# Performance work log

Hardware: AMD Instinct MI355X
Metric: run time of the kernel (lower is better)

Reference implementation:

```python
import jax, jax.numpy as jnp
import numpy as np

V = 100277      # VOCAB_SIZE
SCR = 64        # SCRATCH_SLOTS
STEPS = 8       # MAX_STEPS_LIMIT
H = 8           # num_heads (hard-coded in UniversalReasoner)
NEG = -1e9


def _layernorm(x, s, b, eps=1e-6):
    mu = x.mean(-1, keepdims=True)
    var = ((x - mu) ** 2).mean(-1, keepdims=True)
    return (x - mu) * jax.lax.rsqrt(var + eps) * s + b


def setup_inputs() -> dict:
    key = jax.random.key(0)
    ks = jax.random.split(key, 16)
    D = 1024
    n = lambda k, shape, sc=0.02: jax.random.normal(k, shape, dtype=jnp.float32) * sc
    return {
        "tokens": jax.random.randint(ks[0], (16, 128), 0, V),
        "embed": n(ks[1], (V, D)),
        "time_embed": n(ks[2], (STEPS + 1, D)),
        "scratch": n(ks[3], (1, SCR, D)),
        "wq": n(ks[4], (D, D)), "bq": jnp.zeros((D,), jnp.float32),
        "wk": n(ks[5], (D, D)), "bk": jnp.zeros((D,), jnp.float32),
        "wv": n(ks[6], (D, D)), "bv": jnp.zeros((D,), jnp.float32),
        "wo": n(ks[7], (D, D)), "bo": jnp.zeros((D,), jnp.float32),
        "ln1_s": jnp.ones((D,), jnp.float32), "ln1_b": jnp.zeros((D,), jnp.float32),
        "ln2_s": jnp.ones((D,), jnp.float32), "ln2_b": jnp.zeros((D,), jnp.float32),
        "w1": n(ks[8], (D, 4 * D)), "b1": jnp.zeros((4 * D,), jnp.float32),
        "w2": n(ks[9], (4 * D, D)), "b2": jnp.zeros((D,), jnp.float32),
        "halt_w": n(ks[10], (D, 1)), "halt_b": jnp.zeros((1,), jnp.float32),
        "dec_w": n(ks[11], (D, V)), "dec_b": jnp.zeros((V,), jnp.float32),
    }


def reference(tokens, embed, time_embed, scratch, wq, bq, wk, bk, wv, bv, wo, bo,
              ln1_s, ln1_b, ln2_s, ln2_b, w1, b1, w2, b2, halt_w, halt_b, dec_w, dec_b):
    B, S = tokens.shape
    D = embed.shape[1]
    hd = D // H
    T = S + SCR                     # seq + scratch slots
    scale = hd ** -0.5

    # RoPE caches (matches 10000**(arange(0,hd,2)/hd) in the module)
    inv_freq = 1.0 / 10000.0 ** (jnp.arange(0, hd, 2, dtype=jnp.float32) / hd)
    t = jnp.arange(T, dtype=jnp.float32)
    freqs = jnp.outer(t, inv_freq)              # [T, hd/2]
    sin = jnp.sin(freqs); cos = jnp.cos(freqs)
    sin_ext = jnp.stack([sin, sin], -1).reshape(T, hd)[None, :, None, :]
    cos_ext = jnp.stack([cos, cos], -1).reshape(T, hd)[None, :, None, :]

    # hybrid mask: causal for the seq part, fully-visible rows for scratch tokens
    causal = jnp.tril(jnp.ones((T, T), dtype=bool))
    mask = causal.at[S:, :].set(True)[None, None, :, :]   # [1,1,T,T]

    def rotate(x):  # x: [B,T,H,hd]
        xe, xo = x[..., 0::2], x[..., 1::2]
        xr = jnp.stack([-xo, xe], -1).reshape(x.shape)
        return x * cos_ext + xr * sin_ext

    def block(x):   # one StandardReasoningBlock on [B,T,D]
        h = _layernorm(x, ln1_s, ln1_b)
        q = (h @ wq + bq).reshape(B, T, H, hd)
        k = (h @ wk + bk).reshape(B, T, H, hd)
        v = (h @ wv + bv).reshape(B, T, H, hd)
        q, k = rotate(q), rotate(k)
        logits = jnp.einsum('bshd,bthd->bhst', q, k) * scale
        logits = jnp.where(mask, logits, NEG)
        w = jax.nn.softmax(logits, axis=-1)
        o = jnp.einsum('bhst,bthd->bshd', w, v).reshape(B, T, D)
        x = x + (o @ wo + bo)
        h2 = _layernorm(x, ln2_s, ln2_b)
        x = x + jax.nn.gelu(h2 @ w1 + b1, approximate=True) @ w2 + b2
        return x

    z0 = jnp.concatenate([embed[tokens], jnp.tile(scratch, (B, 1, 1))], axis=1)  # [B,T,D]

    def step(z, i):
        zt = z + time_embed[i][None, None, :]
        nz = block(zt)
        halt = jax.nn.sigmoid((nz[:, S:, :] @ halt_w + halt_b).mean(axis=(1, 2)))  # [B]
        return nz, halt

    final_z, halts = jax.lax.scan(step, z0, jnp.arange(STEPS))   # halts: [STEPS, B]
    logits_out = final_z[:, :S, :] @ dec_w + dec_b               # [B,S,V]
    return logits_out, halts
```

## Files before the change

kernel.cpp:

```cpp
#include <hip/hip_runtime.h>
#include <hip/hip_bf16.h>
#include <math.h>


typedef float  f32x4  __attribute__((ext_vector_type(4)));
typedef __bf16 bf16x8 __attribute__((ext_vector_type(8)));
typedef __bf16 bf16x4 __attribute__((ext_vector_type(4)));

static constexpr int BB   = 16;
static constexpr int S    = 128;
static constexpr int SCR  = 64;
static constexpr int T    = 192;
static constexpr int D    = 1024;
static constexpr int H    = 8;
static constexpr int HD   = 128;
static constexpr int DFF  = 4096;
static constexpr int NSTEP= 8;
static constexpr int V    = 100277;
static constexpr int ROWS = BB * T;
static constexpr int MD   = BB * S;
static constexpr long long LOGITS = (long long)BB * S * V;
static constexpr size_t QSZ = (size_t)BB * H * T * HD;

#define DEV __device__ __forceinline__

DEV void gload16(const __bf16* g, __bf16* l) {
  __builtin_amdgcn_global_load_lds(
      (__attribute__((address_space(1))) void*)(g),
      (__attribute__((address_space(3))) void*)(l), 16, 0, 0);
}

template <int EPI>
__global__ __launch_bounds__(256) void k_gemm(
    const __bf16* __restrict__ A, long long sA, int ldA, int M,
    const __bf16* __restrict__ Bt, long long sB, int ldB, int N, int K,
    const float* __restrict__ bias, void* __restrict__ C, long long sC,
    int ldC, const float* __restrict__ rct, const float* __restrict__ rst) {
  const int bz = blockIdx.z;
  const __bf16* Ab;
  const __bf16* Bb;
  if constexpr (EPI == 4) {
    Ab = A + (size_t)bz * K;
    Bb = Bt + (size_t)bz * K;
  } else {
    Ab = A + (size_t)bz * sA;
    Bb = Bt + (size_t)bz * sB;
  }
  const int tm = blockIdx.y * 128, tn = blockIdx.x * 128;
  const int tid = threadIdx.x;
  const int lane = tid & 63, wv = tid >> 6;
  const int wr = wv >> 1, wc = wv & 1;

  __shared__ __bf16 As[2][128 * 32];
  __shared__ __bf16 Bs[2][128 * 32];

  f32x4 acc[4][4];
#pragma unroll
  for (int m = 0; m < 4; m++)
#pragma unroll
    for (int n = 0; n < 4; n++) acc[m][n] = (f32x4)(0.f);

  const int lrow = lane >> 2;
  const int lcol = (((lane & 3) ^ ((lrow >> 1) & 3)) * 8);
  int arow[2], brow[2];
#pragma unroll
  for (int c2 = 0; c2 < 2; c2++) {
    const int ch = wv * 2 + c2;
    int ar = tm + ch * 16 + lrow; if (ar > M - 1) ar = M - 1;
    int br = tn + ch * 16 + lrow; if (br > N - 1) br = N - 1;
    arow[c2] = ar; brow[c2] = br;
  }

  auto stage = [&](int buf, int kk) {
#pragma unroll
    for (int c2 = 0; c2 < 2; c2++) {
      const int ch = wv * 2 + c2;
      gload16(Ab + (size_t)arow[c2] * ldA + kk + lcol, &As[buf][ch * 512]);
      gload16(Bb + (size_t)brow[c2] * ldB + kk + lcol, &Bs[buf][ch * 512]);
    }
  };

  const int rsl = (((lane >> 4) ^ (((lane & 15) >> 1) & 3)) * 8);
  auto compute = [&](int cur) {
    bf16x8 af[4], bfv[4];
#pragma unroll
    for (int m = 0; m < 4; m++)
      af[m] = *(const bf16x8*)&As[cur][(wr * 64 + m * 16 + (lane & 15)) * 32 + rsl];
#pragma unroll
    for (int n = 0; n < 4; n++)
      bfv[n] = *(const bf16x8*)&Bs[cur][(wc * 64 + n * 16 + (lane & 15)) * 32 + rsl];
    asm volatile("s_waitcnt lgkmcnt(0)" ::: "memory");
    __builtin_amdgcn_sched_barrier(0);
    __builtin_amdgcn_s_barrier();
#pragma unroll
    for (int m = 0; m < 4; m++)
#pragma unroll
      for (int n = 0; n < 4; n++)
        acc[m][n] = __builtin_amdgcn_mfma_f32_16x16x32_bf16(af[m], bfv[n],
                                                            acc[m][n], 0, 0, 0);
  };

  const int niter = K >> 5;
  stage(0, 0);
  for (int it = 0; it < niter - 1; ++it) {
    const int cur = it & 1;
    stage(cur ^ 1, (it + 1) << 5);
    asm volatile("s_waitcnt vmcnt(4)" ::: "memory");
    __builtin_amdgcn_s_barrier();
    compute(cur);
  }
  asm volatile("s_waitcnt vmcnt(0)" ::: "memory");
  __builtin_amdgcn_s_barrier();
  compute((niter - 1) & 1);

  const int r0 = tm + wr * 64, c0 = tn + wc * 64;
  if constexpr (EPI == 5) {
    const int kind = tn >> 10;
#pragma unroll
    for (int n = 0; n < 4; n++) {
      const int c = c0 + n * 16 + (lane & 15);
      const int hh = (c & 1023) >> 7, d = c & 127, jp = d >> 1;
      const float bsv = bias[c];
#pragma unroll
      for (int m = 0; m < 4; m++) {
        const int rb = r0 + m * 16 + ((lane >> 4) << 2);
#pragma unroll
        for (int j = 0; j < 4; j++) {
          const int r = rb + j;
          const float x = acc[m][n][j] + bsv;
          const float xo = __shfl_xor(x, 1);
          const int b = r / T, t = r % T;
          if (kind == 2) {
            ((__bf16*)C)[2 * QSZ + ((size_t)((b * H + hh) * HD + d)) * T + t] =
                (__bf16)x;
          } else {
            const float cs = rct[t * 64 + jp], sn = rst[t * 64 + jp];
            const float o = (c & 1) ? (x * cs + xo * sn) : (x * cs - xo * sn);
            ((__bf16*)C)[(size_t)kind * QSZ +
                         ((size_t)((b * H + hh) * T + t)) * HD + d] = (__bf16)o;
          }
        }
      }
    }
    return;
  }
#pragma unroll
  for (int n = 0; n < 4; n++) {
    const int c = c0 + n * 16 + (lane & 15);
    if (c >= N) continue;
    const float bsv = (bias && (EPI != 4 || bz == 0)) ? bias[c] : 0.f;
#pragma unroll
    for (int m = 0; m < 4; m++) {
      const int rb = r0 + m * 16 + ((lane >> 4) << 2);
#pragma unroll
      for (int j = 0; j < 4; j++) {
        const int r = rb + j;
        if (r >= M) continue;
        float x = acc[m][n][j] + bsv;
        if constexpr (EPI == 3) {
          const int b = bz >> 3, hh = bz & 7;
          ((__bf16*)C)[((size_t)(b * T + r)) * D + hh * HD + c] = (__bf16)x;
        } else if constexpr (EPI == 4) {
          atomicAdd((float*)C + (size_t)r * ldC + c, x);
        } else {
          const size_t idx = (size_t)bz * sC + (size_t)r * ldC + c;
          if constexpr (EPI == 2) {
            const float u = x;
            const float gl =
                0.5f * u * (1.f + tanhf(0.7978845608f * (u + 0.044715f * u * u * u)));
            ((__bf16*)C)[idx] = (__bf16)gl;
          } else if constexpr (EPI == 1) {
            ((float*)C)[idx] += x;
          } else {
            ((float*)C)[idx] = x;
          }
        }
      }
    }
  }
}

static constexpr int DEC_NT = (V + 127) / 128;
static constexpr int DEC_NWG = 16 * DEC_NT;

__global__ __launch_bounds__(256) void k_dec(const __bf16* __restrict__ A,
                                             const __bf16* __restrict__ Bt,
                                             const float* __restrict__ bias,
                                             float* __restrict__ C) {
  const int bid = blockIdx.x;
  const int swz = (bid & 7) * (DEC_NWG / 8) + (bid >> 3);
  const int tm = (swz & 15) * 128, tn = (swz >> 4) * 128;
  const int tid = threadIdx.x;
  const int lane = tid & 63, wv = tid >> 6;
  const int wr = wv >> 1, wc = wv & 1;

  __shared__ __bf16 sAB[2][2][4096];
  float* cbuf = (float*)sAB;

  f32x4 acc[4][4];
#pragma unroll
  for (int m = 0; m < 4; m++)
#pragma unroll
    for (int n = 0; n < 4; n++) acc[m][n] = (f32x4)(0.f);

  const int lrow = lane >> 2;
  const int lcol = (((lane & 3) ^ ((lrow >> 1) & 3)) * 8);
  int arow[2], brow[2];
#pragma unroll
  for (int c2 = 0; c2 < 2; c2++) {
    const int ch = wv * 2 + c2;
    arow[c2] = tm + ch * 16 + lrow;
    int br = tn + ch * 16 + lrow; if (br > V - 1) br = V - 1;
    brow[c2] = br;
  }

  auto stage = [&](int buf, int kk) {
#pragma unroll
    for (int c2 = 0; c2 < 2; c2++) {
      const int ch = wv * 2 + c2;
      gload16(A + (size_t)arow[c2] * D + kk + lcol, &sAB[buf][0][ch * 512]);
      gload16(Bt + (size_t)brow[c2] * D + kk + lcol, &sAB[buf][1][ch * 512]);
    }
  };

  const int rsl = (((lane >> 4) ^ (((lane & 15) >> 1) & 3)) * 8);
  auto compute = [&](int cur) {
    bf16x8 af[4], bfv[4];
#pragma unroll
    for (int m = 0; m < 4; m++)
      af[m] = *(const bf16x8*)&sAB[cur][0][(wr * 64 + m * 16 + (lane & 15)) * 32 + rsl];
#pragma unroll
    for (int n = 0; n < 4; n++)
      bfv[n] = *(const bf16x8*)&sAB[cur][1][(wc * 64 + n * 16 + (lane & 15)) * 32 + rsl];
    asm volatile("s_waitcnt lgkmcnt(0)" ::: "memory");
    __builtin_amdgcn_sched_barrier(0);
    __builtin_amdgcn_s_barrier();
#pragma unroll
    for (int m = 0; m < 4; m++)
#pragma unroll
      for (int n = 0; n < 4; n++)
        acc[m][n] = __builtin_amdgcn_mfma_f32_16x16x32_bf16(af[m], bfv[n],
                                                            acc[m][n], 0, 0, 0);
  };

  stage(0, 0);
  for (int it = 0; it < D / 32 - 1; ++it) {
    const int cur = it & 1;
    stage(cur ^ 1, (it + 1) << 5);
    asm volatile("s_waitcnt vmcnt(4)" ::: "memory");
    __builtin_amdgcn_s_barrier();
    compute(cur);
  }
  asm volatile("s_waitcnt vmcnt(0)" ::: "memory");
  __builtin_amdgcn_s_barrier();
  compute((D / 32 - 1) & 1);
  __syncthreads();

  const int l15 = lane & 15, g4 = lane >> 4;
  const bool full = (tn + 128 <= V);
  for (int pass = 0; pass < 2; ++pass) {
    if (pass) __syncthreads();
    if (wr == pass) {
#pragma unroll
      for (int n = 0; n < 4; n++) {
        const int col = wc * 64 + n * 16 + l15;
        const float bsv = (tn + col < V) ? bias[tn + col] : 0.f;
#pragma unroll
        for (int m = 0; m < 4; m++) {
#pragma unroll
          for (int j = 0; j < 4; j++) {
            const int row = m * 16 + g4 * 4 + j;
            const int slot = (col >> 2) ^ (row & 7);
            cbuf[row * 128 + slot * 4 + (col & 3)] = acc[m][n][j] + bsv;
          }
        }
      }
    }
    __syncthreads();
    const int rbase = tm + pass * 64;
    if (full) {
      const int c8 = tid & 7;
#pragma unroll
      for (int rr = 0; rr < 2; ++rr) {
        const int row = rr * 32 + (tid >> 3);
#pragma unroll
        for (int i = 0; i < 4; ++i) {
          const int ps = (c8 ^ (row & 7)) + i * 8;
          const f32x4 v = *(const f32x4*)&cbuf[row * 128 + ps * 4];
          *(f32x4*)&C[(size_t)(rbase + row) * V + tn + (c8 + i * 8) * 4] = v;
        }
      }
    } else {
      for (int idx = tid; idx < 64 * 128; idx += 256) {
        const int row = idx >> 7, col = idx & 127;
        if (tn + col < V)
          C[(size_t)(rbase + row) * V + tn + col] =
              cbuf[row * 128 + (((col >> 2) ^ (row & 7)) << 2) + (col & 3)];
      }
    }
  }
}

__global__ __launch_bounds__(256) void k_transpose(const float* __restrict__ in,
                                                   __bf16* __restrict__ out,
                                                   int R, int C) {
  __shared__ __bf16 tile[32][33];
  const int c0 = blockIdx.x * 32, r0 = blockIdx.y * 32;
  const int tx = threadIdx.x & 31, ty = threadIdx.x >> 5;
#pragma unroll
  for (int i = 0; i < 32; i += 8) {
    const int r = r0 + ty + i, c = c0 + tx;
    tile[ty + i][tx] = (r < R && c < C) ? (__bf16)in[(size_t)r * C + c] : (__bf16)0.f;
  }
  __syncthreads();
  const int oc = threadIdx.x >> 3, rch = (threadIdx.x & 7) * 4;
  const int occ = c0 + oc, orr = r0 + rch;
  if (occ < C && orr + 3 < R) {
    bf16x4 v;
#pragma unroll
    for (int j = 0; j < 4; j++) v[j] = tile[rch + j][oc];
    *(bf16x4*)(out + (size_t)occ * R + orr) = v;
  }
}

__global__ __launch_bounds__(256) void k_concat_bias(const float* bq,
                                                     const float* bk,
                                                     const float* bv,
                                                     float* out) {
  const int i = blockIdx.x * 256 + threadIdx.x;
  if (i < D) { out[i] = bq[i]; out[D + i] = bk[i]; out[2 * D + i] = bv[i]; }
}

__global__ __launch_bounds__(256) void k_rope_table(float* __restrict__ ct,
                                                    float* __restrict__ st) {
  const int i = blockIdx.x * 256 + threadIdx.x;
  if (i < T * 64) {
    const int t = i >> 6, j = i & 63;
    const float inv = expf(-((float)(2 * j) * (1.f / 128.f)) * 9.210340371976184f);
    const float ang = (float)t * inv;
    ct[i] = cosf(ang);
    st[i] = sinf(ang);
  }
}

__global__ __launch_bounds__(256) void k_build_z(const int* __restrict__ tokens,
                                                 const float* __restrict__ embed,
                                                 const float* __restrict__ scratch,
                                                 float* __restrict__ z) {
  const int row = blockIdx.x;
  const int b = row / T, t = row % T;
  const float* src = (t < S) ? embed + (size_t)tokens[b * S + t] * D
                             : scratch + (size_t)(t - S) * D;
  ((float4*)(z + (size_t)row * D))[threadIdx.x] =
      ((const float4*)src)[threadIdx.x];
}

template <bool ADDT>
__global__ __launch_bounds__(256) void k_ln(float* __restrict__ z,
                                            const float* __restrict__ te,
                                            const float* __restrict__ gs,
                                            const float* __restrict__ gb,
                                            __bf16* __restrict__ h) {
  const int row = blockIdx.x, tid = threadIdx.x;
  float* zp = z + (size_t)row * D;
  float4 x = ((float4*)zp)[tid];
  if (ADDT) {
    const float4 t4 = ((const float4*)te)[tid];
    x.x += t4.x; x.y += t4.y; x.z += t4.z; x.w += t4.w;
    ((float4*)zp)[tid] = x;
  }
  float s = x.x + x.y + x.z + x.w;
  float s2 = x.x * x.x + x.y * x.y + x.z * x.z + x.w * x.w;
#pragma unroll
  for (int o = 32; o; o >>= 1) { s += __shfl_xor(s, o); s2 += __shfl_xor(s2, o); }
  __shared__ float rs[4], rq[4];
  const int wv = tid >> 6, ln = tid & 63;
  if (!ln) { rs[wv] = s; rq[wv] = s2; }
  __syncthreads();
  s = rs[0] + rs[1] + rs[2] + rs[3];
  s2 = rq[0] + rq[1] + rq[2] + rq[3];
  const float mu = s * (1.f / D);
  const float var = s2 * (1.f / D) - mu * mu;
  const float rinv = 1.0f / sqrtf(var + 1e-6f);
  const int c = tid * 4;
  const float4 g4 = ((const float4*)gs)[tid];
  const float4 b4 = ((const float4*)gb)[tid];
  bf16x4 o4;
  o4[0] = (__bf16)((x.x - mu) * rinv * g4.x + b4.x);
  o4[1] = (__bf16)((x.y - mu) * rinv * g4.y + b4.y);
  o4[2] = (__bf16)((x.z - mu) * rinv * g4.z + b4.z);
  o4[3] = (__bf16)((x.w - mu) * rinv * g4.w + b4.w);
  *(bf16x4*)(h + (size_t)row * D + c) = o4;
}

__global__ __launch_bounds__(256) void k_softmax(const float* __restrict__ sc,
                                                 __bf16* __restrict__ P) {
  const int wv = threadIdx.x >> 6, lane = threadIdx.x & 63;
  const int row = blockIdx.x * 4 + wv;
  const int tq = row % T;
  const int kmax = (tq < S) ? (tq + 1) : T;
  const float* srow = sc + (size_t)row * T;
  float v[3];
#pragma unroll
  for (int jj = 0; jj < 3; jj++) {
    const int idx = lane + 64 * jj;
    v[jj] = (idx < kmax) ? srow[idx] * 0.08838834764831845f : -1e30f;
  }
  float m = fmaxf(v[0], fmaxf(v[1], v[2]));
#pragma unroll
  for (int o = 32; o; o >>= 1) m = fmaxf(m, __shfl_xor(m, o));
  float e[3], ssum = 0.f;
#pragma unroll
  for (int jj = 0; jj < 3; jj++) { e[jj] = expf(v[jj] - m); ssum += e[jj]; }
#pragma unroll
  for (int o = 32; o; o >>= 1) ssum += __shfl_xor(ssum, o);
  const float inv = 1.f / ssum;
#pragma unroll
  for (int jj = 0; jj < 3; jj++)
    P[(size_t)row * T + lane + 64 * jj] = (__bf16)(e[jj] * inv);
}

__global__ __launch_bounds__(256) void k_halt(const float* __restrict__ z,
                                              const float* __restrict__ hw,
                                              const float* __restrict__ hb,
                                              float* __restrict__ out) {
  const int b = blockIdx.x, tid = threadIdx.x;
  const float4 w4 = ((const float4*)hw)[tid];
  float acc = 0.f;
  for (int j = 0; j < SCR; j++) {
    const float4 x = ((const float4*)(z + ((size_t)(b * T + S + j)) * D))[tid];
    acc += x.x * w4.x + x.y * w4.y + x.z * w4.z + x.w * w4.w;
  }
#pragma unroll
  for (int o = 32; o; o >>= 1) acc += __shfl_xor(acc, o);
  __shared__ float rs[4];
  const int wv = tid >> 6, ln = tid & 63;
  if (!ln) rs[wv] = acc;
  __syncthreads();
  if (tid == 0) {
    const float tot = rs[0] + rs[1] + rs[2] + rs[3];
    out[b] = 1.f / (1.f + expf(-(tot * (1.f / SCR) + hb[0])));
  }
}

__global__ __launch_bounds__(256) void k_cast(const float* __restrict__ z,
                                              __bf16* __restrict__ zb) {
  const int row = blockIdx.x;
  const int b = row >> 7, s = row & 127;
  const float4 x = ((const float4*)(z + ((size_t)(b * T + s)) * D))[threadIdx.x];
  bf16x4 o;
  o[0] = (__bf16)x.x; o[1] = (__bf16)x.y; o[2] = (__bf16)x.z; o[3] = (__bf16)x.w;
  *(bf16x4*)(zb + (size_t)row * D + threadIdx.x * 4) = o;
}

extern "C" void kernel_launch(void* const* d_in, const int* in_sizes, int n_in,
                              void* d_out, int out_size, void* d_ws,
                              size_t ws_size, hipStream_t stream) {
  const int* tokens = (const int*)d_in[0];
  const float* embed = (const float*)d_in[1];
  const float* time_embed = (const float*)d_in[2];
  const float* scratch = (const float*)d_in[3];
  const float* wq = (const float*)d_in[4];  const float* bq = (const float*)d_in[5];
  const float* wk = (const float*)d_in[6];  const float* bk = (const float*)d_in[7];
  const float* wvv = (const float*)d_in[8]; const float* bv = (const float*)d_in[9];
  const float* wo = (const float*)d_in[10]; const float* bo = (const float*)d_in[11];
  const float* ln1s = (const float*)d_in[12]; const float* ln1b = (const float*)d_in[13];
  const float* ln2s = (const float*)d_in[14]; const float* ln2b = (const float*)d_in[15];
  const float* w1 = (const float*)d_in[16]; const float* b1 = (const float*)d_in[17];
  const float* w2 = (const float*)d_in[18]; const float* b2 = (const float*)d_in[19];
  const float* hw = (const float*)d_in[20]; const float* hb = (const float*)d_in[21];
  const float* dw = (const float*)d_in[22]; const float* db = (const float*)d_in[23];

  char* w = (char*)d_ws;
  size_t off = 0;
  auto al = [&](size_t n) { size_t o = off; off += (n + 255) & ~(size_t)255; return o; };
  const size_t oWqkvT = al((size_t)3 * D * D * 2);
  const size_t oWoT   = al((size_t)D * D * 2);
  const size_t oW1T   = al((size_t)DFF * D * 2);
  const size_t oW2T   = al((size_t)D * DFF * 2);
  const size_t oDecT  = al((size_t)V * D * 2);
  const size_t oBqkv  = al((size_t)3 * D * 4);
  const size_t oCt    = al((size_t)T * 64 * 4);
  const size_t oSt    = al((size_t)T * 64 * 4);
  const size_t oZ     = al((size_t)ROWS * D * 4);
  const size_t oH     = al((size_t)ROWS * D * 2);
  const size_t oG     = al((size_t)ROWS * DFF * 2);
  const size_t oOB    = al((size_t)ROWS * D * 2);
  const size_t oQ     = al(QSZ * 2);
  const size_t oK     = al(QSZ * 2);
  const size_t oVT    = al(QSZ * 2);
  const size_t oSc    = al((size_t)BB * H * T * T * 4);
  const size_t oP     = al((size_t)BB * H * T * T * 2);
  (void)ws_size; (void)in_sizes; (void)n_in; (void)out_size;

  __bf16* WqkvT = (__bf16*)(w + oWqkvT);
  __bf16* WoT   = (__bf16*)(w + oWoT);
  __bf16* W1T   = (__bf16*)(w + oW1T);
  __bf16* W2T   = (__bf16*)(w + oW2T);
  __bf16* DecT  = (__bf16*)(w + oDecT);
  float*  bqkv  = (float*)(w + oBqkv);
  float*  ct    = (float*)(w + oCt);
  float*  st    = (float*)(w + oSt);
  float*  z     = (float*)(w + oZ);
  __bf16* h     = (__bf16*)(w + oH);
  __bf16* g     = (__bf16*)(w + oG);
  __bf16* ob    = (__bf16*)(w + oOB);
  __bf16* qb    = (__bf16*)(w + oQ);
  __bf16* kb    = (__bf16*)(w + oK);
  __bf16* vT    = (__bf16*)(w + oVT);
  float*  sc    = (float*)(w + oSc);
  __bf16* P     = (__bf16*)(w + oP);
  __bf16* zb    = (__bf16*)(w + oH);

  float* logits = (float*)d_out;
  float* halts  = (float*)d_out + LOGITS;

  k_transpose<<<dim3(32, 32), 256, 0, stream>>>(wq, WqkvT, D, D);
  k_transpose<<<dim3(32, 32), 256, 0, stream>>>(wk, WqkvT + (size_t)D * D, D, D);
  k_transpose<<<dim3(32, 32), 256, 0, stream>>>(wvv, WqkvT + (size_t)2 * D * D, D, D);
  k_transpose<<<dim3(32, 32), 256, 0, stream>>>(wo, WoT, D, D);
  k_transpose<<<dim3(128, 32), 256, 0, stream>>>(w1, W1T, D, DFF);
  k_transpose<<<dim3(32, 128), 256, 0, stream>>>(w2, W2T, DFF, D);
  k_transpose<<<dim3((V + 31) / 32, 32), 256, 0, stream>>>(dw, DecT, D, V);
  k_concat_bias<<<4, 256, 0, stream>>>(bq, bk, bv, bqkv);
  k_rope_table<<<(T * 64 + 255) / 256, 256, 0, stream>>>(ct, st);
  k_build_z<<<ROWS, 256, 0, stream>>>(tokens, embed, scratch, z);

  for (int step = 0; step < NSTEP; step++) {
    k_ln<true><<<ROWS, 256, 0, stream>>>(z, time_embed + (size_t)step * D, ln1s, ln1b, h);
    k_gemm<5><<<dim3(24, 24, 1), 256, 0, stream>>>(h, 0, D, ROWS, WqkvT, 0, D,
                                                   3 * D, D, bqkv, qb, 0, 0, ct, st);
    k_gemm<0><<<dim3(2, 2, BB * H), 256, 0, stream>>>(
        qb, (long long)T * HD, HD, T, kb, (long long)T * HD, HD, T, HD, nullptr,
        sc, (long long)T * T, T, nullptr, nullptr);
    k_softmax<<<BB * H * T / 4, 256, 0, stream>>>(sc, P);
    k_gemm<3><<<dim3(1, 2, BB * H), 256, 0, stream>>>(
        P, (long long)T * T, T, T, vT, (long long)HD * T, T, HD, T, nullptr,
        ob, 0, 0, nullptr, nullptr);
    k_gemm<1><<<dim3(8, 24, 1), 256, 0, stream>>>(ob, 0, D, ROWS, WoT, 0, D, D,
                                                  D, bo, z, 0, D, nullptr, nullptr);
    k_ln<false><<<ROWS, 256, 0, stream>>>(z, nullptr, ln2s, ln2b, h);
    k_gemm<2><<<dim3(32, 24, 1), 256, 0, stream>>>(h, 0, D, ROWS, W1T, 0, D,
                                                   DFF, D, b1, g, 0, DFF, nullptr, nullptr);
    k_gemm<4><<<dim3(8, 24, 4), 256, 0, stream>>>(g, 0, DFF, ROWS, W2T, 0, DFF,
                                                  D, DFF / 4, b2, z, 0, D, nullptr, nullptr);
    k_halt<<<BB, 256, 0, stream>>>(z, hw, hb, halts + step * BB);
  }

  k_cast<<<MD, 256, 0, stream>>>(z, zb);
  k_dec<<<DEC_NWG, 256, 0, stream>>>(zb, DecT, db, logits);
}
```

Before: 3.105 ms.

## Fuse QK^T, masked softmax and PV into one attention kernel per head

Replaces the three-kernel attention path (score GEMM, softmax, PV GEMM) with a single kernel per (batch, head). The kernel keeps Q fragments in registers, stages K and V^T in swizzled LDS, computes masked softmax in registers and writes P to LDS before the PV MFMA. This removes the fp32 score and bf16 probability round trips through global memory and two launches per step. It also makes the decoder logits stores nontemporal. The cost is only 128 workgroups, which underfills the GPU, and 120 KB of dynamic LDS per block.

```diff
diff --git a/kernel.cpp b/kernel.cpp
--- a/kernel.cpp
+++ b/kernel.cpp
@@ -157,10 +157,7 @@
         const int r = rb + j;
         if (r >= M) continue;
         float x = acc[m][n][j] + bsv;
-        if constexpr (EPI == 3) {
-          const int b = bz >> 3, hh = bz & 7;
-          ((__bf16*)C)[((size_t)(b * T + r)) * D + hh * HD + c] = (__bf16)x;
-        } else if constexpr (EPI == 4) {
+        if constexpr (EPI == 4) {
           atomicAdd((float*)C + (size_t)r * ldC + c, x);
         } else {
           const size_t idx = (size_t)bz * sC + (size_t)r * ldC + c;
@@ -169,15 +166,159 @@
             const float gl =
                 0.5f * u * (1.f + tanhf(0.7978845608f * (u + 0.044715f * u * u * u)));
             ((__bf16*)C)[idx] = (__bf16)gl;
-          } else if constexpr (EPI == 1) {
+          } else {
             ((float*)C)[idx] += x;
-          } else {
-            ((float*)C)[idx] = x;
           }
         }
       }
     }
   }
+}
+
+__global__ __launch_bounds__(256) void k_attn(const __bf16* __restrict__ qb,
+                                              const __bf16* __restrict__ kb,
+                                              const __bf16* __restrict__ vT,
+                                              __bf16* __restrict__ ob) {
+  extern __shared__ char smem[];
+  __bf16* Kl = (__bf16*)smem;
+  __bf16* Pl = (__bf16*)smem;
+  __bf16* Vl = (__bf16*)(smem + 73728);
+  const int bh = blockIdx.x;
+  const int tid = threadIdx.x, lane = tid & 63, wv = tid >> 6;
+  const int g4 = lane >> 4, l15 = lane & 15;
+  const size_t hoff = (size_t)bh * T * HD;
+  const size_t voff = (size_t)bh * HD * T;
+
+  bf16x8 qf[3][4];
+#pragma unroll
+  for (int m = 0; m < 3; m++)
+#pragma unroll
+    for (int ks = 0; ks < 4; ks++) {
+      const int tq = wv * 48 + m * 16 + l15;
+      qf[m][ks] = *(const bf16x8*)(qb + hoff + (size_t)tq * HD + ks * 32 + g4 * 8);
+    }
+
+#pragma unroll
+  for (int ci = 0; ci < 12; ci++) {
+    const int ch = wv * 12 + ci;
+    const int grow = ch * 4 + g4;
+    const int sl = l15 ^ (grow & 7);
+    gload16(kb + hoff + (size_t)grow * HD + sl * 8, Kl + ch * 512);
+  }
+#pragma unroll
+  for (int ci = 0; ci < 12; ci++) {
+    const int ch = wv * 12 + ci;
+    const int c = ch >> 4, ch2 = ch & 15;
+    const int d = ch2 * 8 + (lane >> 3);
+    const int sl = (lane & 7) ^ (d & 7);
+    gload16(vT + voff + (size_t)d * T + c * 64 + sl * 8,
+            Vl + c * 8192 + ch2 * 512);
+  }
+  asm volatile("s_waitcnt vmcnt(0)" ::: "memory");
+  __builtin_amdgcn_s_barrier();
+
+  f32x4 sacc[3][12];
+#pragma unroll
+  for (int m = 0; m < 3; m++)
+#pragma unroll
+    for (int nf = 0; nf < 12; nf++) sacc[m][nf] = (f32x4)(0.f);
+#pragma unroll
+  for (int ks = 0; ks < 4; ks++)
+#pragma unroll
+    for (int nf = 0; nf < 12; nf++) {
+      const int row = nf * 16 + l15;
+      const int sl = (ks * 4 + g4) ^ (row & 7);
+      const bf16x8 kf = *(const bf16x8*)&Kl[row * 128 + sl * 8];
+#pragma unroll
+      for (int m = 0; m < 3; m++)
+        sacc[m][nf] = __builtin_amdgcn_mfma_f32_16x16x32_bf16(qf[m][ks], kf,
+                                                              sacc[m][nf], 0, 0, 0);
+    }
+
+  const float scale = 0.08838834764831845f;
+  float inv[3][4];
+#pragma unroll
+  for (int m = 0; m < 3; m++)
+#pragma unroll
+    for (int j = 0; j < 4; j++) {
+      const int tq = wv * 48 + m * 16 + g4 * 4 + j;
+#pragma unroll
+      for (int nf = 0; nf < 12; nf++) {
+        const int c = nf * 16 + l15;
+        float v = sacc[m][nf][j] * scale;
+        if (tq < S && c > tq) v = -1e30f;
+        sacc[m][nf][j] = v;
+      }
+      float mm = -1e30f;
+#pragma unroll
+      for (int nf = 0; nf < 12; nf++) mm = fmaxf(mm, sacc[m][nf][j]);
+#pragma unroll
+      for (int o = 1; o < 16; o <<= 1) mm = fmaxf(mm, __shfl_xor(mm, o));
+      float sum = 0.f;
+#pragma unroll
+      for (int nf = 0; nf < 12; nf++) {
+        const float e = __expf(sacc[m][nf][j] - mm);
+        sacc[m][nf][j] = e;
+        sum += e;
+      }
+#pragma unroll
+      for (int o = 1; o < 16; o <<= 1) sum += __shfl_xor(sum, o);
+      inv[m][j] = 1.f / sum;
+    }
+
+  __builtin_amdgcn_s_barrier();
+#pragma unroll
+  for (int m = 0; m < 3; m++)
+#pragma unroll
+    for (int nf = 0; nf < 12; nf++)
+#pragma unroll
+      for (int j = 0; j < 4; j++) {
+        const int q = wv * 48 + m * 16 + g4 * 4 + j;
+        const int c = nf * 16 + l15;
+        Pl[q * 192 + (((c >> 3) ^ (q & 7)) * 8) + (c & 7)] =
+            (__bf16)(sacc[m][nf][j] * inv[m][j]);
+      }
+  asm volatile("s_waitcnt lgkmcnt(0)" ::: "memory");
+  __builtin_amdgcn_sched_barrier(0);
+
+  f32x4 oacc[3][8];
+#pragma unroll
+  for (int m = 0; m < 3; m++)
+#pragma unroll
+    for (int nf = 0; nf < 8; nf++) oacc[m][nf] = (f32x4)(0.f);
+#pragma unroll
+  for (int ks = 0; ks < 6; ks++) {
+    bf16x8 pf[3];
+#pragma unroll
+    for (int m = 0; m < 3; m++) {
+      const int q = wv * 48 + m * 16 + l15;
+      const int sl = (ks * 4 + g4) ^ (q & 7);
+      pf[m] = *(const bf16x8*)&Pl[q * 192 + sl * 8];
+    }
+#pragma unroll
+    for (int nf = 0; nf < 8; nf++) {
+      const int d = nf * 16 + l15;
+      const int sl = ((ks & 1) * 4 + g4) ^ (d & 7);
+      const bf16x8 vf = *(const bf16x8*)&Vl[(ks >> 1) * 8192 + d * 64 + sl * 8];
+#pragma unroll
+      for (int m = 0; m < 3; m++)
+        oacc[m][nf] = __builtin_amdgcn_mfma_f32_16x16x32_bf16(pf[m], vf,
+                                                              oacc[m][nf], 0, 0, 0);
+    }
+  }
+
+  const int b = bh >> 3, hh = bh & 7;
+#pragma unroll
+  for (int m = 0; m < 3; m++)
+#pragma unroll
+    for (int nf = 0; nf < 8; nf++) {
+      const int d = nf * 16 + l15;
+#pragma unroll
+      for (int j = 0; j < 4; j++) {
+        const int tq = wv * 48 + m * 16 + g4 * 4 + j;
+        ob[((size_t)(b * T + tq)) * D + hh * HD + d] = (__bf16)oacc[m][nf][j];
+      }
+    }
 }
 
 static constexpr int DEC_NT = (V + 127) / 128;
@@ -287,15 +428,17 @@
         for (int i = 0; i < 4; ++i) {
           const int ps = (c8 ^ (row & 7)) + i * 8;
           const f32x4 v = *(const f32x4*)&cbuf[row * 128 + ps * 4];
-          *(f32x4*)&C[(size_t)(rbase + row) * V + tn + (c8 + i * 8) * 4] = v;
+          __builtin_nontemporal_store(
+              v, (f32x4*)&C[(size_t)(rbase + row) * V + tn + (c8 + i * 8) * 4]);
         }
       }
     } else {
       for (int idx = tid; idx < 64 * 128; idx += 256) {
         const int row = idx >> 7, col = idx & 127;
         if (tn + col < V)
-          C[(size_t)(rbase + row) * V + tn + col] =
-              cbuf[row * 128 + (((col >> 2) ^ (row & 7)) << 2) + (col & 3)];
+          __builtin_nontemporal_store(
+              cbuf[row * 128 + (((col >> 2) ^ (row & 7)) << 2) + (col & 3)],
+              &C[(size_t)(rbase + row) * V + tn + col]);
       }
     }
   }
@@ -393,33 +536,6 @@
   *(bf16x4*)(h + (size_t)row * D + c) = o4;
 }
 
-__global__ __launch_bounds__(256) void k_softmax(const float* __restrict__ sc,
-                                                 __bf16* __restrict__ P) {
-  const int wv = threadIdx.x >> 6, lane = threadIdx.x & 63;
-  const int row = blockIdx.x * 4 + wv;
-  const int tq = row % T;
-  const int kmax = (tq < S) ? (tq + 1) : T;
-  const float* srow = sc + (size_t)row * T;
-  float v[3];
-#pragma unroll
-  for (int jj = 0; jj < 3; jj++) {
-    const int idx = lane + 64 * jj;
-    v[jj] = (idx < kmax) ? srow[idx] * 0.08838834764831845f : -1e30f;
-  }
-  float m = fmaxf(v[0], fmaxf(v[1], v[2]));
-#pragma unroll
-  for (int o = 32; o; o >>= 1) m = fmaxf(m, __shfl_xor(m, o));
-  float e[3], ssum = 0.f;
-#pragma unroll
-  for (int jj = 0; jj < 3; jj++) { e[jj] = expf(v[jj] - m); ssum += e[jj]; }
-#pragma unroll
-  for (int o = 32; o; o >>= 1) ssum += __shfl_xor(ssum, o);
-  const float inv = 1.f / ssum;
-#pragma unroll
-  for (int jj = 0; jj < 3; jj++)
-    P[(size_t)row * T + lane + 64 * jj] = (__bf16)(e[jj] * inv);
-}
-
 __global__ __launch_bounds__(256) void k_halt(const float* __restrict__ z,
                                               const float* __restrict__ hw,
                                               const float* __restrict__ hb,
@@ -489,8 +605,6 @@
   const size_t oQ     = al(QSZ * 2);
   const size_t oK     = al(QSZ * 2);
   const size_t oVT    = al(QSZ * 2);
-  const size_t oSc    = al((size_t)BB * H * T * T * 4);
-  const size_t oP     = al((size_t)BB * H * T * T * 2);
   (void)ws_size; (void)in_sizes; (void)n_in; (void)out_size;
 
   __bf16* WqkvT = (__bf16*)(w + oWqkvT);
@@ -508,8 +622,6 @@
   __bf16* qb    = (__bf16*)(w + oQ);
   __bf16* kb    = (__bf16*)(w + oK);
   __bf16* vT    = (__bf16*)(w + oVT);
-  float*  sc    = (float*)(w + oSc);
-  __bf16* P     = (__bf16*)(w + oP);
   __bf16* zb    = (__bf16*)(w + oH);
 
   float* logits = (float*)d_out;
@@ -530,13 +642,7 @@
     k_ln<true><<<ROWS, 256, 0, stream>>>(z, time_embed + (size_t)step * D, ln1s, ln1b, h);
     k_gemm<5><<<dim3(24, 24, 1), 256, 0, stream>>>(h, 0, D, ROWS, WqkvT, 0, D,
                                                    3 * D, D, bqkv, qb, 0, 0, ct, st);
-    k_gemm<0><<<dim3(2, 2, BB * H), 256, 0, stream>>>(
-        qb, (long long)T * HD, HD, T, kb, (long long)T * HD, HD, T, HD, nullptr,
-        sc, (long long)T * T, T, nullptr, nullptr);
-    k_softmax<<<BB * H * T / 4, 256, 0, stream>>>(sc, P);
-    k_gemm<3><<<dim3(1, 2, BB * H), 256, 0, stream>>>(
-        P, (long long)T * T, T, T, vT, (long long)HD * T, T, HD, T, nullptr,
-        ob, 0, 0, nullptr, nullptr);
+    k_attn<<<BB * H, 256, 122880, stream>>>(qb, kb, vT, ob);
     k_gemm<1><<<dim3(8, 24, 1), 256, 0, stream>>>(ob, 0, D, ROWS, WoT, 0, D, D,
                                                   D, bo, z, 0, D, nullptr, nullptr);
     k_ln<false><<<ROWS, 256, 0, stream>>>(z, nullptr, ln2s, ln2b, h);
```

Measured after the change: 2.956 ms. 4.8% less time.
